# Performance work log

Measured on AMD Instinct MI355X. Metric: run time of the kernel, lower is better.

The kernel has to match this reference:

```python
import jax, jax.numpy as jnp
import numpy as np

B, T, D, H = 8, 4096, 256, 256

def setup_inputs() -> dict:
    key = jax.random.key(0)
    ks = jax.random.split(key, 6)
    scale = 1.0 / np.sqrt(D)
    return {
        "x": jax.random.normal(ks[0], (B, T, D), dtype=jnp.float32),
        "h0": jax.random.normal(ks[1], (B, H), dtype=jnp.float32),
        "Wz": jax.random.normal(ks[2], (H, D), dtype=jnp.float32) * scale,
        "bz": jax.random.normal(ks[3], (H,), dtype=jnp.float32) * scale,
        "Wh": jax.random.normal(ks[4], (H, D), dtype=jnp.float32) * scale,
        "bh": jax.random.normal(ks[5], (H,), dtype=jnp.float32) * scale,
    }

def reference(x, h0, Wz, bz, Wh, bh):
    # gate and update depend only on the input (minGRU): compute in one shot
    gate = jax.nn.sigmoid(jnp.einsum("btd,hd->bth", x, Wz) + bz)   # [B,T,H]
    update = jnp.einsum("btd,hd->bth", x, Wh) + bh                  # [B,T,H]

    def step(h, gu):
        g, u = gu
        h_new = (1.0 - g) * h + g * u
        return h_new, h_new

    # scan over time; xs laid out [T,B,H]
    _, hs = jax.lax.scan(step, h0, (jnp.swapaxes(gate, 0, 1), jnp.swapaxes(update, 0, 1)))
    return jnp.swapaxes(hs, 0, 1)  # [B,T,H]
```

## Files before the change

### kernel.cpp

```cpp
#include <hip/hip_runtime.h>
#include <hip/hip_fp16.h>


namespace {
constexpr int kB  = 8;
constexpr int kT  = 4096;
constexpr int kD  = 256;
constexpr int kH  = 256;
constexpr int kBT = kB * kT;

constexpr int TM  = 128;
constexpr int TH  = 64;
constexpr int BK  = 64;
constexpr int kNT = kT / TM;
constexpr int kNChain = kB * (kH / TH);
constexpr int EPS = 66;
}

typedef short s16x8 __attribute__((ext_vector_type(8)));
typedef short s16x4 __attribute__((ext_vector_type(4)));
typedef float f32x4 __attribute__((ext_vector_type(4)));

__device__ __forceinline__ short f2bf(float f) {
    union { float f; unsigned int u; } v; v.f = f;
    unsigned int r = v.u + 0x7fffu + ((v.u >> 16) & 1u);
    return (short)(r >> 16);
}

__device__ __forceinline__ unsigned int cvt_pk_bf16(float lo, float hi) {
    unsigned int r;
    asm("v_cvt_pk_bf16_f32 %0, %1, %2" : "=v"(r) : "v"(lo), "v"(hi));
    return r;
}

__device__ __forceinline__ void load_lds16(const void* g, void* l) {
    __builtin_amdgcn_global_load_lds(
        (const __attribute__((address_space(1))) void*)g,
        (__attribute__((address_space(3))) void*)l, 16, 0, 0);
}

__global__ __launch_bounds__(256)
void prep(const float* __restrict__ Wz,
          const float* __restrict__ Wh,
          unsigned short* __restrict__ wzb,
          unsigned short* __restrict__ whb,
          float4* __restrict__ aggz)
{
    constexpr int W4 = kH * kD / 4;
    const int i = blockIdx.x * 256 + threadIdx.x;

    if (i >= 2 * W4) {
        float4 z; z.x = 0.f; z.y = 0.f; z.z = 0.f; z.w = 0.f;
        aggz[i - 2 * W4] = z;
        return;
    }
    const float* src; unsigned short* dst; int j;
    if (i < W4) { src = Wz; dst = wzb; j = i; }
    else        { src = Wh; dst = whb; j = i - W4; }
    const float4 v = ((const float4*)src)[j];
    s16x4 p;
    p[0] = f2bf(v.x); p[1] = f2bf(v.y); p[2] = f2bf(v.z); p[3] = f2bf(v.w);
    ((s16x4*)dst)[j] = p;
}

__global__ __launch_bounds__(256, 4)
void gemm_scan_fused(const float* __restrict__ x,
                     const unsigned short* __restrict__ wzb,
                     const unsigned short* __restrict__ whb,
                     const float* __restrict__ bz,
                     const float* __restrict__ bh,
                     const float* __restrict__ h0,
                     unsigned long long* __restrict__ agg,
                     float* __restrict__ out)
{
    __shared__ __align__(16) unsigned char smem[36096];
    unsigned short* Xs  = (unsigned short*)smem;
    unsigned short* Wzs = Xs  + 128 * 64;
    unsigned short* Whs = Wzs + 64 * 64;
    __half* a_lds   = (__half*)smem;
    __half* b_lds   = a_lds + 128 * EPS;
    float2* sub_lds = (float2*)(smem + 33792);
    float*  hs_lds  = (float*)(smem + 35840);

    const int tid  = threadIdx.x;
    const int lane = tid & 63;
    const int wv   = tid >> 6;
    const int ln15 = lane & 15;
    const int quad = lane >> 4;
    const int wr0  = (wv & 1) * 64;
    const int wc0  = (wv >> 1) * 32;

    const int id  = blockIdx.x;
    const int r8  = id & 7;
    const int q   = id >> 3;
    const int cg  = q & 3;
    const int bt  = (q >> 2) * 8 + r8;
    const int b   = bt >> 5;
    const int t   = bt & 31;
    const int chain = b * 4 + cg;
    const int col0  = cg * TH;
    const int row0  = b * kT + t * TM;

    const int srow = lane >> 3;
    const int swslot = (lane & 7) ^ srow;

    f32x4 accZ[4][2] = {};
    f32x4 accU[4][2] = {};

    for (int k0 = 0; k0 < kD; k0 += BK) {
        #pragma unroll
        for (int s = 0; s < 2; ++s) {
            const int seg = wv * 2 + s;
            const int m = seg * 8 + srow;
            load_lds16(wzb + (size_t)(col0 + m) * kD + k0 + swslot * 8,
                       Wzs + seg * 512);
            load_lds16(whb + (size_t)(col0 + m) * kD + k0 + swslot * 8,
                       Whs + seg * 512);
        }
        #pragma unroll
        for (int j = 0; j < 4; ++j) {
            const int bi  = j * 256 + tid;
            const int r   = bi >> 3;
            const int blk = bi & 7;
            const float* src = x + (size_t)(row0 + r) * kD + k0 + blk * 8;
            const float4 v0 = *(const float4*)src;
            const float4 v1 = *(const float4*)(src + 4);
            union { unsigned int u[4]; s16x8 v; } pk;
            pk.u[0] = cvt_pk_bf16(v0.x, v0.y);
            pk.u[1] = cvt_pk_bf16(v0.z, v0.w);
            pk.u[2] = cvt_pk_bf16(v1.x, v1.y);
            pk.u[3] = cvt_pk_bf16(v1.z, v1.w);
            *(s16x8*)&Xs[r * 64 + ((blk ^ (r & 7)) << 3)] = pk.v;
        }
        __syncthreads();

        #pragma unroll
        for (int kk = 0; kk < BK; kk += 32) {
            const int bblk = (kk >> 3) + quad;
            s16x8 af[4], bzf[2], buf[2];
            #pragma unroll
            for (int mt = 0; mt < 4; ++mt) {
                const int r = wr0 + mt * 16 + ln15;
                af[mt] = *(const s16x8*)&Xs[r * 64 + ((bblk ^ (r & 7)) << 3)];
            }
            #pragma unroll
            for (int nt = 0; nt < 2; ++nt) {
                const int rw = wc0 + nt * 16 + ln15;
                const int so = (bblk ^ (rw & 7)) << 3;
                bzf[nt] = *(const s16x8*)&Wzs[rw * 64 + so];
                buf[nt] = *(const s16x8*)&Whs[rw * 64 + so];
            }
            #pragma unroll
            for (int mt = 0; mt < 4; ++mt) {
                #pragma unroll
                for (int nt = 0; nt < 2; ++nt) {
                    accZ[mt][nt] = __builtin_amdgcn_mfma_f32_16x16x32_bf16(
                        af[mt], bzf[nt], accZ[mt][nt], 0, 0, 0);
                    accU[mt][nt] = __builtin_amdgcn_mfma_f32_16x16x32_bf16(
                        af[mt], buf[nt], accU[mt][nt], 0, 0, 0);
                }
            }
        }
        __syncthreads();
    }

    #pragma unroll
    for (int nt = 0; nt < 2; ++nt) {
        const int col = col0 + wc0 + nt * 16 + ln15;
        const int lc  = wc0 + nt * 16 + ln15;
        const float bzv = bz[col];
        const float bhv = bh[col];
        #pragma unroll
        for (int mt = 0; mt < 4; ++mt) {
            const int rb = wr0 + mt * 16 + quad * 4;
            #pragma unroll
            for (int r = 0; r < 4; ++r) {
                const float z = accZ[mt][nt][r] + bzv;
                const float g = 1.0f / (1.0f + __expf(-z));
                const float u = accU[mt][nt][r] + bhv;
                a_lds[(rb + r) * EPS + lc] = __float2half_rn(1.0f - g);
                b_lds[(rb + r) * EPS + lc] = __float2half_rn(g * u);
            }
        }
    }
    __syncthreads();

    const int s = tid >> 6;
    const int h = tid & 63;
    {
        float A = 1.0f, Bv = 0.0f;
        #pragma unroll 8
        for (int r = s * 32; r < s * 32 + 32; ++r) {
            const float a  = __half2float(a_lds[r * EPS + h]);
            const float bb = __half2float(b_lds[r * EPS + h]);
            Bv = fmaf(a, Bv, bb);
            A *= a;
        }
        float2 o; o.x = A; o.y = Bv;
        sub_lds[s * 64 + h] = o;
    }
    __syncthreads();

    if (tid < 64) {
        float A = 1.0f, Bv = 0.0f;
        #pragma unroll
        for (int s2 = 0; s2 < 4; ++s2) {
            const float2 g = sub_lds[s2 * 64 + tid];
            Bv = fmaf(g.x, Bv, g.y);
            A *= g.x;
        }
        union { float2 f; unsigned long long u; } pk;
        pk.f.x = A; pk.f.y = Bv;
        pk.u |= 1ull;
        __hip_atomic_store(&agg[(size_t)(chain * kNT + t) * 64 + tid], pk.u,
                           __ATOMIC_RELAXED, __HIP_MEMORY_SCOPE_AGENT);

        float hs = h0[(size_t)b * kH + col0 + tid];
        for (int j0 = 0; j0 < t; j0 += 8) {
            const int nb = (t - j0 < 8) ? (t - j0) : 8;
            unsigned long long u[8];
            #pragma unroll
            for (int q2 = 0; q2 < 8; ++q2)
                if (q2 < nb)
                    u[q2] = __hip_atomic_load(
                        &agg[(size_t)(chain * kNT + j0 + q2) * 64 + tid],
                        __ATOMIC_RELAXED, __HIP_MEMORY_SCOPE_AGENT);
            #pragma unroll
            for (int q2 = 0; q2 < 8; ++q2) {
                if (q2 < nb) {
                    while (u[q2] == 0ull)
                        u[q2] = __hip_atomic_load(
                            &agg[(size_t)(chain * kNT + j0 + q2) * 64 + tid],
                            __ATOMIC_RELAXED, __HIP_MEMORY_SCOPE_AGENT);
                    union { unsigned long long u; float2 f; } qk; qk.u = u[q2];
                    hs = fmaf(qk.f.x, hs, qk.f.y);
                }
            }
        }
        hs_lds[tid] = hs;
    }
    __syncthreads();

    {
        float hv = hs_lds[h];
        #pragma unroll
        for (int s2 = 0; s2 < s; ++s2) {
            const float2 g = sub_lds[s2 * 64 + h];
            hv = fmaf(g.x, hv, g.y);
        }
        #pragma unroll 8
        for (int r = 0; r < 32; ++r) {
            const int lr = s * 32 + r;
            const float a  = __half2float(a_lds[lr * EPS + h]);
            const float bb = __half2float(b_lds[lr * EPS + h]);
            hv = fmaf(a, hv, bb);
            __builtin_nontemporal_store(hv, &out[(size_t)(row0 + lr) * kH + col0 + h]);
        }
    }
}

extern "C" void kernel_launch(void* const* d_in, const int* in_sizes, int n_in,
                              void* d_out, int out_size, void* d_ws, size_t ws_size,
                              hipStream_t stream)
{
    const float* x  = (const float*)d_in[0];
    const float* h0 = (const float*)d_in[1];
    const float* Wz = (const float*)d_in[2];
    const float* bz = (const float*)d_in[3];
    const float* Wh = (const float*)d_in[4];
    const float* bh = (const float*)d_in[5];
    float* out = (float*)d_out;

    unsigned char* ws = (unsigned char*)d_ws;
    unsigned short* wzb = (unsigned short*)ws;   ws += (size_t)kH * kD * 2;
    unsigned short* whb = (unsigned short*)ws;   ws += (size_t)kH * kD * 2;
    unsigned long long* agg = (unsigned long long*)ws;

    constexpr int PREP_ITEMS = 2 * (kH * kD / 4)
                             + kNChain * kNT * TH * 8 / 16;
    prep<<<PREP_ITEMS / 256, 256, 0, stream>>>(
        Wz, Wh, wzb, whb, (float4*)agg);
    gemm_scan_fused<<<kNChain * kNT, 256, 0, stream>>>(
        x, wzb, whb, bz, bh, h0, agg, out);
}
```

Measured before the change: 113.6 us.

## Load GEMM operands directly from global into registers, bypassing LDS staging

Removes the LDS-staged tiling of x and the bf16 weights in the fused GEMM+scan kernel. Each lane now loads its MFMA fragments straight from global memory into registers, with a register double buffer that prefetches the next k-slice while the current one is computed. This drops the __syncthreads barriers and LDS traffic, and s_setprio is raised around the MFMA block. In exchange, x rows are re-read by the waves that share them, accesses are less coalesced, register use grows, and occupancy is lowered to 3 blocks per SM.

```diff
diff --git a/kernel.cpp b/kernel.cpp
--- a/kernel.cpp
+++ b/kernel.cpp
@@ -11,7 +11,6 @@
 
 constexpr int TM  = 128;
 constexpr int TH  = 64;
-constexpr int BK  = 64;
 constexpr int kNT = kT / TM;
 constexpr int kNChain = kB * (kH / TH);
 constexpr int EPS = 66;
@@ -31,12 +30,6 @@
     unsigned int r;
     asm("v_cvt_pk_bf16_f32 %0, %1, %2" : "=v"(r) : "v"(lo), "v"(hi));
     return r;
-}
-
-__device__ __forceinline__ void load_lds16(const void* g, void* l) {
-    __builtin_amdgcn_global_load_lds(
-        (const __attribute__((address_space(1))) void*)g,
-        (__attribute__((address_space(3))) void*)l, 16, 0, 0);
 }
 
 __global__ __launch_bounds__(256)
@@ -63,7 +56,7 @@
     ((s16x4*)dst)[j] = p;
 }
 
-__global__ __launch_bounds__(256, 4)
+__global__ __launch_bounds__(256, 3)
 void gemm_scan_fused(const float* __restrict__ x,
                      const unsigned short* __restrict__ wzb,
                      const unsigned short* __restrict__ whb,
@@ -74,9 +67,6 @@
                      float* __restrict__ out)
 {
     __shared__ __align__(16) unsigned char smem[36096];
-    unsigned short* Xs  = (unsigned short*)smem;
-    unsigned short* Wzs = Xs  + 128 * 64;
-    unsigned short* Whs = Wzs + 64 * 64;
     __half* a_lds   = (__half*)smem;
     __half* b_lds   = a_lds + 128 * EPS;
     float2* sub_lds = (float2*)(smem + 33792);
@@ -101,67 +91,68 @@
     const int col0  = cg * TH;
     const int row0  = b * kT + t * TM;
 
-    const int srow = lane >> 3;
-    const int swslot = (lane & 7) ^ srow;
-
     f32x4 accZ[4][2] = {};
     f32x4 accU[4][2] = {};
 
-    for (int k0 = 0; k0 < kD; k0 += BK) {
-        #pragma unroll
-        for (int s = 0; s < 2; ++s) {
-            const int seg = wv * 2 + s;
-            const int m = seg * 8 + srow;
-            load_lds16(wzb + (size_t)(col0 + m) * kD + k0 + swslot * 8,
-                       Wzs + seg * 512);
-            load_lds16(whb + (size_t)(col0 + m) * kD + k0 + swslot * 8,
-                       Whs + seg * 512);
-        }
-        #pragma unroll
-        for (int j = 0; j < 4; ++j) {
-            const int bi  = j * 256 + tid;
-            const int r   = bi >> 3;
-            const int blk = bi & 7;
-            const float* src = x + (size_t)(row0 + r) * kD + k0 + blk * 8;
-            const float4 v0 = *(const float4*)src;
-            const float4 v1 = *(const float4*)(src + 4);
+    const float* xbase = x + (size_t)(row0 + wr0 + ln15) * kD + quad * 8;
+    const unsigned short* wzbase = wzb + (size_t)(col0 + wc0 + ln15) * kD + quad * 8;
+    const unsigned short* whbase = whb + (size_t)(col0 + wc0 + ln15) * kD + quad * 8;
+
+    float4 cxa[4], cxb[4];
+    s16x8  wzr[2][2], whr[2][2];
+
+    #pragma unroll
+    for (int mt = 0; mt < 4; ++mt) {
+        const float* p = xbase + (size_t)mt * 16 * kD;
+        cxa[mt] = *(const float4*)p;
+        cxb[mt] = *(const float4*)(p + 4);
+    }
+    #pragma unroll
+    for (int nt = 0; nt < 2; ++nt) {
+        wzr[0][nt] = *(const s16x8*)(wzbase + (size_t)nt * 16 * kD);
+        whr[0][nt] = *(const s16x8*)(whbase + (size_t)nt * 16 * kD);
+    }
+
+    #pragma unroll
+    for (int st = 0; st < 8; ++st) {
+        s16x8 af[4];
+        #pragma unroll
+        for (int mt = 0; mt < 4; ++mt) {
             union { unsigned int u[4]; s16x8 v; } pk;
-            pk.u[0] = cvt_pk_bf16(v0.x, v0.y);
-            pk.u[1] = cvt_pk_bf16(v0.z, v0.w);
-            pk.u[2] = cvt_pk_bf16(v1.x, v1.y);
-            pk.u[3] = cvt_pk_bf16(v1.z, v1.w);
-            *(s16x8*)&Xs[r * 64 + ((blk ^ (r & 7)) << 3)] = pk.v;
-        }
-        __syncthreads();
-
-        #pragma unroll
-        for (int kk = 0; kk < BK; kk += 32) {
-            const int bblk = (kk >> 3) + quad;
-            s16x8 af[4], bzf[2], buf[2];
+            pk.u[0] = cvt_pk_bf16(cxa[mt].x, cxa[mt].y);
+            pk.u[1] = cvt_pk_bf16(cxa[mt].z, cxa[mt].w);
+            pk.u[2] = cvt_pk_bf16(cxb[mt].x, cxb[mt].y);
+            pk.u[3] = cvt_pk_bf16(cxb[mt].z, cxb[mt].w);
+            af[mt] = pk.v;
+        }
+        if (st < 7) {
+            const int o = (st + 1) * 32;
             #pragma unroll
             for (int mt = 0; mt < 4; ++mt) {
-                const int r = wr0 + mt * 16 + ln15;
-                af[mt] = *(const s16x8*)&Xs[r * 64 + ((bblk ^ (r & 7)) << 3)];
+                const float* p = xbase + (size_t)mt * 16 * kD + o;
+                cxa[mt] = *(const float4*)p;
+                cxb[mt] = *(const float4*)(p + 4);
             }
             #pragma unroll
             for (int nt = 0; nt < 2; ++nt) {
-                const int rw = wc0 + nt * 16 + ln15;
-                const int so = (bblk ^ (rw & 7)) << 3;
-                bzf[nt] = *(const s16x8*)&Wzs[rw * 64 + so];
-                buf[nt] = *(const s16x8*)&Whs[rw * 64 + so];
-            }
-            #pragma unroll
-            for (int mt = 0; mt < 4; ++mt) {
-                #pragma unroll
-                for (int nt = 0; nt < 2; ++nt) {
-                    accZ[mt][nt] = __builtin_amdgcn_mfma_f32_16x16x32_bf16(
-                        af[mt], bzf[nt], accZ[mt][nt], 0, 0, 0);
-                    accU[mt][nt] = __builtin_amdgcn_mfma_f32_16x16x32_bf16(
-                        af[mt], buf[nt], accU[mt][nt], 0, 0, 0);
-                }
-            }
-        }
-        __syncthreads();
+                wzr[(st + 1) & 1][nt] =
+                    *(const s16x8*)(wzbase + (size_t)nt * 16 * kD + o);
+                whr[(st + 1) & 1][nt] =
+                    *(const s16x8*)(whbase + (size_t)nt * 16 * kD + o);
+            }
+        }
+        __builtin_amdgcn_s_setprio(1);
+        #pragma unroll
+        for (int mt = 0; mt < 4; ++mt) {
+            #pragma unroll
+            for (int nt = 0; nt < 2; ++nt) {
+                accZ[mt][nt] = __builtin_amdgcn_mfma_f32_16x16x32_bf16(
+                    af[mt], wzr[st & 1][nt], accZ[mt][nt], 0, 0, 0);
+                accU[mt][nt] = __builtin_amdgcn_mfma_f32_16x16x32_bf16(
+                    af[mt], whr[st & 1][nt], accU[mt][nt], 0, 0, 0);
+            }
+        }
+        __builtin_amdgcn_s_setprio(0);
     }
 
     #pragma unroll
```

Measured after the change: 147.3 us. +29.7%, slower.

## Halve time tile, process two tiles per block with carried state and prefetch

Applied to the files above, without the earlier changes.

Shrinks the time tile to 64 rows and has each block handle two tiles, the second being 32 tiles later in the same chain. For the second tile the block starts the serial lookback from its own first tile's result, so it only scans the tiles in between. The K loop now prefetches the next x slice into registers and double-buffers the weights in LDS, and MFMA issue gets higher wave priority. This aims to shorten the decoupled-lookback chain and overlap global loads with compute, at the cost of more barriers and larger LDS use per block.

```diff
diff --git a/kernel.cpp b/kernel.cpp
--- a/kernel.cpp
+++ b/kernel.cpp
@@ -7,13 +7,12 @@
 constexpr int kT  = 4096;
 constexpr int kD  = 256;
 constexpr int kH  = 256;
-constexpr int kBT = kB * kT;
-
-constexpr int TM  = 128;
+
+constexpr int TM  = 64;
 constexpr int TH  = 64;
 constexpr int BK  = 64;
-constexpr int kNT = kT / TM;
-constexpr int kNChain = kB * (kH / TH);
+constexpr int kTilesPC = kT / TM;
+constexpr int kNChain  = kB * (kH / TH);
 constexpr int EPS = 66;
 }
 
@@ -73,189 +72,246 @@
                      unsigned long long* __restrict__ agg,
                      float* __restrict__ out)
 {
-    __shared__ __align__(16) unsigned char smem[36096];
-    unsigned short* Xs  = (unsigned short*)smem;
-    unsigned short* Wzs = Xs  + 128 * 64;
-    unsigned short* Whs = Wzs + 64 * 64;
+    __shared__ __align__(16) unsigned char smem[40960];
+    unsigned short* Xs = (unsigned short*)smem;
     __half* a_lds   = (__half*)smem;
-    __half* b_lds   = a_lds + 128 * EPS;
-    float2* sub_lds = (float2*)(smem + 33792);
-    float*  hs_lds  = (float*)(smem + 35840);
+    __half* b_lds   = a_lds + 64 * EPS;
+    float2* sub_lds = (float2*)(smem + 16896);
+    float*  hs_lds  = (float*)(smem + 18944);
 
     const int tid  = threadIdx.x;
     const int lane = tid & 63;
     const int wv   = tid >> 6;
     const int ln15 = lane & 15;
     const int quad = lane >> 4;
-    const int wr0  = (wv & 1) * 64;
+    const int wr0  = (wv & 1) * 32;
     const int wc0  = (wv >> 1) * 32;
 
     const int id  = blockIdx.x;
     const int r8  = id & 7;
     const int q   = id >> 3;
     const int cg  = q & 3;
-    const int bt  = (q >> 2) * 8 + r8;
-    const int b   = bt >> 5;
-    const int t   = bt & 31;
+    const int idx = (q >> 2) * 8 + r8;
+    const int b   = idx >> 5;
+    const int j   = idx & 31;
     const int chain = b * 4 + cg;
     const int col0  = cg * TH;
-    const int row0  = b * kT + t * TM;
 
     const int srow = lane >> 3;
     const int swslot = (lane & 7) ^ srow;
-
-    f32x4 accZ[4][2] = {};
-    f32x4 accU[4][2] = {};
-
-    for (int k0 = 0; k0 < kD; k0 += BK) {
-        #pragma unroll
-        for (int s = 0; s < 2; ++s) {
-            const int seg = wv * 2 + s;
+    const int xr   = tid >> 3;
+    const int xblk = tid & 7;
+
+    float carry = 0.f;
+
+    for (int rnd = 0; rnd < 2; ++rnd) {
+        const int t    = j + rnd * 32;
+        const int row0 = b * kT + t * TM;
+
+        f32x4 accZ[2][2] = {};
+        f32x4 accU[2][2] = {};
+        float4 xv0[2], xv1[2];
+
+        #pragma unroll
+        for (int jj = 0; jj < 2; ++jj) {
+            const int r = jj * 32 + xr;
+            const float* p = x + (size_t)(row0 + r) * kD + xblk * 8;
+            xv0[jj] = *(const float4*)p;
+            xv1[jj] = *(const float4*)(p + 4);
+        }
+        #pragma unroll
+        for (int s2 = 0; s2 < 2; ++s2) {
+            const int seg = wv * 2 + s2;
             const int m = seg * 8 + srow;
-            load_lds16(wzb + (size_t)(col0 + m) * kD + k0 + swslot * 8,
-                       Wzs + seg * 512);
-            load_lds16(whb + (size_t)(col0 + m) * kD + k0 + swslot * 8,
-                       Whs + seg * 512);
-        }
-        #pragma unroll
-        for (int j = 0; j < 4; ++j) {
-            const int bi  = j * 256 + tid;
-            const int r   = bi >> 3;
-            const int blk = bi & 7;
-            const float* src = x + (size_t)(row0 + r) * kD + k0 + blk * 8;
-            const float4 v0 = *(const float4*)src;
-            const float4 v1 = *(const float4*)(src + 4);
+            load_lds16(wzb + (size_t)(col0 + m) * kD + swslot * 8,
+                       smem + 8192 + seg * 1024);
+            load_lds16(whb + (size_t)(col0 + m) * kD + swslot * 8,
+                       smem + 16384 + seg * 1024);
+        }
+        #pragma unroll
+        for (int jj = 0; jj < 2; ++jj) {
+            const int r = jj * 32 + xr;
             union { unsigned int u[4]; s16x8 v; } pk;
-            pk.u[0] = cvt_pk_bf16(v0.x, v0.y);
-            pk.u[1] = cvt_pk_bf16(v0.z, v0.w);
-            pk.u[2] = cvt_pk_bf16(v1.x, v1.y);
-            pk.u[3] = cvt_pk_bf16(v1.z, v1.w);
-            *(s16x8*)&Xs[r * 64 + ((blk ^ (r & 7)) << 3)] = pk.v;
-        }
-        __syncthreads();
-
-        #pragma unroll
-        for (int kk = 0; kk < BK; kk += 32) {
-            const int bblk = (kk >> 3) + quad;
-            s16x8 af[4], bzf[2], buf[2];
+            pk.u[0] = cvt_pk_bf16(xv0[jj].x, xv0[jj].y);
+            pk.u[1] = cvt_pk_bf16(xv0[jj].z, xv0[jj].w);
+            pk.u[2] = cvt_pk_bf16(xv1[jj].x, xv1[jj].y);
+            pk.u[3] = cvt_pk_bf16(xv1[jj].z, xv1[jj].w);
+            *(s16x8*)&Xs[r * 64 + ((xblk ^ (r & 7)) << 3)] = pk.v;
+        }
+        __syncthreads();
+
+        #pragma unroll
+        for (int k = 0; k < 4; ++k) {
+            if (k < 3) {
+                const int o = (k + 1) * BK;
+                #pragma unroll
+                for (int jj = 0; jj < 2; ++jj) {
+                    const int r = jj * 32 + xr;
+                    const float* p = x + (size_t)(row0 + r) * kD + o + xblk * 8;
+                    xv0[jj] = *(const float4*)p;
+                    xv1[jj] = *(const float4*)(p + 4);
+                }
+                unsigned char* wn = smem + 8192 + (((k + 1) & 1) ? 16384 : 0);
+                #pragma unroll
+                for (int s2 = 0; s2 < 2; ++s2) {
+                    const int seg = wv * 2 + s2;
+                    const int m = seg * 8 + srow;
+                    load_lds16(wzb + (size_t)(col0 + m) * kD + o + swslot * 8,
+                               wn + seg * 1024);
+                    load_lds16(whb + (size_t)(col0 + m) * kD + o + swslot * 8,
+                               wn + 8192 + seg * 1024);
+                }
+            }
+            __builtin_amdgcn_sched_barrier(0);
+
+            const unsigned short* Wzc =
+                (const unsigned short*)(smem + 8192 + ((k & 1) ? 16384 : 0));
+            const unsigned short* Whc = Wzc + 4096;
             #pragma unroll
-            for (int mt = 0; mt < 4; ++mt) {
-                const int r = wr0 + mt * 16 + ln15;
-                af[mt] = *(const s16x8*)&Xs[r * 64 + ((bblk ^ (r & 7)) << 3)];
-            }
+            for (int kk = 0; kk < BK; kk += 32) {
+                const int bblk = (kk >> 3) + quad;
+                s16x8 af[2], bzf[2], bhf[2];
+                #pragma unroll
+                for (int mt = 0; mt < 2; ++mt) {
+                    const int r = wr0 + mt * 16 + ln15;
+                    af[mt] = *(const s16x8*)&Xs[r * 64 + ((bblk ^ (r & 7)) << 3)];
+                }
+                #pragma unroll
+                for (int nt = 0; nt < 2; ++nt) {
+                    const int rw = wc0 + nt * 16 + ln15;
+                    const int so = (bblk ^ (rw & 7)) << 3;
+                    bzf[nt] = *(const s16x8*)&Wzc[rw * 64 + so];
+                    bhf[nt] = *(const s16x8*)&Whc[rw * 64 + so];
+                }
+                __builtin_amdgcn_s_setprio(1);
+                #pragma unroll
+                for (int mt = 0; mt < 2; ++mt) {
+                    #pragma unroll
+                    for (int nt = 0; nt < 2; ++nt) {
+                        accZ[mt][nt] = __builtin_amdgcn_mfma_f32_16x16x32_bf16(
+                            af[mt], bzf[nt], accZ[mt][nt], 0, 0, 0);
+                        accU[mt][nt] = __builtin_amdgcn_mfma_f32_16x16x32_bf16(
+                            af[mt], bhf[nt], accU[mt][nt], 0, 0, 0);
+                    }
+                }
+                __builtin_amdgcn_s_setprio(0);
+            }
+            __syncthreads();
+
+            if (k < 3) {
+                #pragma unroll
+                for (int jj = 0; jj < 2; ++jj) {
+                    const int r = jj * 32 + xr;
+                    union { unsigned int u[4]; s16x8 v; } pk;
+                    pk.u[0] = cvt_pk_bf16(xv0[jj].x, xv0[jj].y);
+                    pk.u[1] = cvt_pk_bf16(xv0[jj].z, xv0[jj].w);
+                    pk.u[2] = cvt_pk_bf16(xv1[jj].x, xv1[jj].y);
+                    pk.u[3] = cvt_pk_bf16(xv1[jj].z, xv1[jj].w);
+                    *(s16x8*)&Xs[r * 64 + ((xblk ^ (r & 7)) << 3)] = pk.v;
+                }
+                __syncthreads();
+            }
+        }
+
+        #pragma unroll
+        for (int nt = 0; nt < 2; ++nt) {
+            const int col = col0 + wc0 + nt * 16 + ln15;
+            const int lc  = wc0 + nt * 16 + ln15;
+            const float bzv = bz[col];
+            const float bhv = bh[col];
             #pragma unroll
-            for (int nt = 0; nt < 2; ++nt) {
-                const int rw = wc0 + nt * 16 + ln15;
-                const int so = (bblk ^ (rw & 7)) << 3;
-                bzf[nt] = *(const s16x8*)&Wzs[rw * 64 + so];
-                buf[nt] = *(const s16x8*)&Whs[rw * 64 + so];
-            }
+            for (int mt = 0; mt < 2; ++mt) {
+                const int rb = wr0 + mt * 16 + quad * 4;
+                #pragma unroll
+                for (int r = 0; r < 4; ++r) {
+                    const float z = accZ[mt][nt][r] + bzv;
+                    const float g = 1.0f / (1.0f + __expf(-z));
+                    const float u = accU[mt][nt][r] + bhv;
+                    a_lds[(rb + r) * EPS + lc] = __float2half_rn(1.0f - g);
+                    b_lds[(rb + r) * EPS + lc] = __float2half_rn(g * u);
+                }
+            }
+        }
+        __syncthreads();
+
+        const int s = tid >> 6;
+        const int h = tid & 63;
+        {
+            float A = 1.0f, Bv = 0.0f;
+            #pragma unroll 8
+            for (int r = s * 16; r < s * 16 + 16; ++r) {
+                const float a  = __half2float(a_lds[r * EPS + h]);
+                const float bb = __half2float(b_lds[r * EPS + h]);
+                Bv = fmaf(a, Bv, bb);
+                A *= a;
+            }
+            float2 o; o.x = A; o.y = Bv;
+            sub_lds[s * 64 + h] = o;
+        }
+        __syncthreads();
+
+        if (tid < 64) {
+            float A = 1.0f, Bv = 0.0f;
             #pragma unroll
-            for (int mt = 0; mt < 4; ++mt) {
-                #pragma unroll
-                for (int nt = 0; nt < 2; ++nt) {
-                    accZ[mt][nt] = __builtin_amdgcn_mfma_f32_16x16x32_bf16(
-                        af[mt], bzf[nt], accZ[mt][nt], 0, 0, 0);
-                    accU[mt][nt] = __builtin_amdgcn_mfma_f32_16x16x32_bf16(
-                        af[mt], buf[nt], accU[mt][nt], 0, 0, 0);
-                }
-            }
-        }
-        __syncthreads();
-    }
-
-    #pragma unroll
-    for (int nt = 0; nt < 2; ++nt) {
-        const int col = col0 + wc0 + nt * 16 + ln15;
-        const int lc  = wc0 + nt * 16 + ln15;
-        const float bzv = bz[col];
-        const float bhv = bh[col];
-        #pragma unroll
-        for (int mt = 0; mt < 4; ++mt) {
-            const int rb = wr0 + mt * 16 + quad * 4;
+            for (int s2 = 0; s2 < 4; ++s2) {
+                const float2 g = sub_lds[s2 * 64 + tid];
+                Bv = fmaf(g.x, Bv, g.y);
+                A *= g.x;
+            }
+            union { float2 f; unsigned long long u; } pk;
+            pk.f.x = A; pk.f.y = Bv;
+            pk.u |= 1ull;
+            __hip_atomic_store(&agg[(size_t)(chain * kTilesPC + t) * 64 + tid],
+                               pk.u, __ATOMIC_RELAXED, __HIP_MEMORY_SCOPE_AGENT);
+
+            float hs;
+            int p0;
+            if (rnd == 0) { hs = h0[(size_t)b * kH + col0 + tid]; p0 = 0; }
+            else          { hs = carry;                            p0 = j + 1; }
+            for (; p0 < t; p0 += 8) {
+                const int nb = (t - p0 < 8) ? (t - p0) : 8;
+                unsigned long long u[8];
+                #pragma unroll
+                for (int q2 = 0; q2 < 8; ++q2)
+                    if (q2 < nb)
+                        u[q2] = __hip_atomic_load(
+                            &agg[(size_t)(chain * kTilesPC + p0 + q2) * 64 + tid],
+                            __ATOMIC_RELAXED, __HIP_MEMORY_SCOPE_AGENT);
+                #pragma unroll
+                for (int q2 = 0; q2 < 8; ++q2) {
+                    if (q2 < nb) {
+                        while (u[q2] == 0ull)
+                            u[q2] = __hip_atomic_load(
+                                &agg[(size_t)(chain * kTilesPC + p0 + q2) * 64 + tid],
+                                __ATOMIC_RELAXED, __HIP_MEMORY_SCOPE_AGENT);
+                        union { unsigned long long u; float2 f; } qk; qk.u = u[q2];
+                        hs = fmaf(qk.f.x, hs, qk.f.y);
+                    }
+                }
+            }
+            hs_lds[tid] = hs;
+            if (rnd == 0) carry = fmaf(A, hs, Bv);
+        }
+        __syncthreads();
+
+        {
+            float hv = hs_lds[h];
             #pragma unroll
-            for (int r = 0; r < 4; ++r) {
-                const float z = accZ[mt][nt][r] + bzv;
-                const float g = 1.0f / (1.0f + __expf(-z));
-                const float u = accU[mt][nt][r] + bhv;
-                a_lds[(rb + r) * EPS + lc] = __float2half_rn(1.0f - g);
-                b_lds[(rb + r) * EPS + lc] = __float2half_rn(g * u);
-            }
-        }
-    }
-    __syncthreads();
-
-    const int s = tid >> 6;
-    const int h = tid & 63;
-    {
-        float A = 1.0f, Bv = 0.0f;
-        #pragma unroll 8
-        for (int r = s * 32; r < s * 32 + 32; ++r) {
-            const float a  = __half2float(a_lds[r * EPS + h]);
-            const float bb = __half2float(b_lds[r * EPS + h]);
-            Bv = fmaf(a, Bv, bb);
-            A *= a;
-        }
-        float2 o; o.x = A; o.y = Bv;
-        sub_lds[s * 64 + h] = o;
-    }
-    __syncthreads();
-
-    if (tid < 64) {
-        float A = 1.0f, Bv = 0.0f;
-        #pragma unroll
-        for (int s2 = 0; s2 < 4; ++s2) {
-            const float2 g = sub_lds[s2 * 64 + tid];
-            Bv = fmaf(g.x, Bv, g.y);
-            A *= g.x;
-        }
-        union { float2 f; unsigned long long u; } pk;
-        pk.f.x = A; pk.f.y = Bv;
-        pk.u |= 1ull;
-        __hip_atomic_store(&agg[(size_t)(chain * kNT + t) * 64 + tid], pk.u,
-                           __ATOMIC_RELAXED, __HIP_MEMORY_SCOPE_AGENT);
-
-        float hs = h0[(size_t)b * kH + col0 + tid];
-        for (int j0 = 0; j0 < t; j0 += 8) {
-            const int nb = (t - j0 < 8) ? (t - j0) : 8;
-            unsigned long long u[8];
-            #pragma unroll
-            for (int q2 = 0; q2 < 8; ++q2)
-                if (q2 < nb)
-                    u[q2] = __hip_atomic_load(
-                        &agg[(size_t)(chain * kNT + j0 + q2) * 64 + tid],
-                        __ATOMIC_RELAXED, __HIP_MEMORY_SCOPE_AGENT);
-            #pragma unroll
-            for (int q2 = 0; q2 < 8; ++q2) {
-                if (q2 < nb) {
-                    while (u[q2] == 0ull)
-                        u[q2] = __hip_atomic_load(
-                            &agg[(size_t)(chain * kNT + j0 + q2) * 64 + tid],
-                            __ATOMIC_RELAXED, __HIP_MEMORY_SCOPE_AGENT);
-                    union { unsigned long long u; float2 f; } qk; qk.u = u[q2];
-                    hs = fmaf(qk.f.x, hs, qk.f.y);
-                }
-            }
-        }
-        hs_lds[tid] = hs;
-    }
-    __syncthreads();
-
-    {
-        float hv = hs_lds[h];
-        #pragma unroll
-        for (int s2 = 0; s2 < s; ++s2) {
-            const float2 g = sub_lds[s2 * 64 + h];
-            hv = fmaf(g.x, hv, g.y);
-        }
-        #pragma unroll 8
-        for (int r = 0; r < 32; ++r) {
-            const int lr = s * 32 + r;
-            const float a  = __half2float(a_lds[lr * EPS + h]);
-            const float bb = __half2float(b_lds[lr * EPS + h]);
-            hv = fmaf(a, hv, bb);
-            __builtin_nontemporal_store(hv, &out[(size_t)(row0 + lr) * kH + col0 + h]);
-        }
+            for (int s2 = 0; s2 < s; ++s2) {
+                const float2 g = sub_lds[s2 * 64 + h];
+                hv = fmaf(g.x, hv, g.y);
+            }
+            #pragma unroll 8
+            for (int r = 0; r < 16; ++r) {
+                const int lr = s * 16 + r;
+                const float a  = __half2float(a_lds[lr * EPS + h]);
+                const float bb = __half2float(b_lds[lr * EPS + h]);
+                hv = fmaf(a, hv, bb);
+                __builtin_nontemporal_store(
+                    hv, &out[(size_t)(row0 + lr) * kH + col0 + h]);
+            }
+        }
+        __syncthreads();
     }
 }
 
@@ -277,9 +333,9 @@
     unsigned long long* agg = (unsigned long long*)ws;
 
     constexpr int PREP_ITEMS = 2 * (kH * kD / 4)
-                             + kNChain * kNT * TH * 8 / 16;
+                             + kNChain * kTilesPC * 64 * 8 / 16;
     prep<<<PREP_ITEMS / 256, 256, 0, stream>>>(
         Wz, Wh, wzb, whb, (float4*)agg);
-    gemm_scan_fused<<<kNChain * kNT, 256, 0, stream>>>(
+    gemm_scan_fused<<<kNChain * 32, 256, 0, stream>>>(
         x, wzb, whb, bz, bh, h0, agg, out);
 }
```

Result: slower. 132.8 us (+16.9%).

## Pre-convert x to bf16 in prologue and double-buffer async LDS loads in GEMM

Applied to the files above, without the earlier changes.

The prologue kernel now converts the whole input x to bf16 in workspace alongside the weights. The fused GEMM then loads x tiles straight into LDS via global_load_lds instead of doing in-kernel float loads and conversion. The K loop uses BK=32 with double-buffered LDS, prefetching the next tile while computing the current one, and raises wave priority around the MFMAs. This aims to overlap memory with compute and cut per-block conversion work. The cost is an extra full pass writing and re-reading x in bf16, which adds global traffic before the main kernel, since each x element is reused by four column-group blocks.

```diff
diff --git a/kernel.cpp b/kernel.cpp
--- a/kernel.cpp
+++ b/kernel.cpp
@@ -11,7 +11,7 @@
 
 constexpr int TM  = 128;
 constexpr int TH  = 64;
-constexpr int BK  = 64;
+constexpr int BK  = 32;
 constexpr int kNT = kT / TM;
 constexpr int kNChain = kB * (kH / TH);
 constexpr int EPS = 66;
@@ -27,12 +27,6 @@
     return (short)(r >> 16);
 }
 
-__device__ __forceinline__ unsigned int cvt_pk_bf16(float lo, float hi) {
-    unsigned int r;
-    asm("v_cvt_pk_bf16_f32 %0, %1, %2" : "=v"(r) : "v"(lo), "v"(hi));
-    return r;
-}
-
 __device__ __forceinline__ void load_lds16(const void* g, void* l) {
     __builtin_amdgcn_global_load_lds(
         (const __attribute__((address_space(1))) void*)g,
@@ -40,23 +34,27 @@
 }
 
 __global__ __launch_bounds__(256)
-void prep(const float* __restrict__ Wz,
-          const float* __restrict__ Wh,
-          unsigned short* __restrict__ wzb,
-          unsigned short* __restrict__ whb,
-          float4* __restrict__ aggz)
+void prologue(const float* __restrict__ x,
+              const float* __restrict__ Wz,
+              const float* __restrict__ Wh,
+              unsigned short* __restrict__ xbg,
+              unsigned short* __restrict__ wzb,
+              unsigned short* __restrict__ whb,
+              float4* __restrict__ aggz)
 {
-    constexpr int W4 = kH * kD / 4;
+    constexpr int X4 = kBT * kD / 4;
+    constexpr int W4 = kH  * kD / 4;
     const int i = blockIdx.x * 256 + threadIdx.x;
 
-    if (i >= 2 * W4) {
+    if (i >= X4 + 2 * W4) {
         float4 z; z.x = 0.f; z.y = 0.f; z.z = 0.f; z.w = 0.f;
-        aggz[i - 2 * W4] = z;
+        aggz[i - (X4 + 2 * W4)] = z;
         return;
     }
     const float* src; unsigned short* dst; int j;
-    if (i < W4) { src = Wz; dst = wzb; j = i; }
-    else        { src = Wh; dst = whb; j = i - W4; }
+    if (i < X4)           { src = x;  dst = xbg; j = i; }
+    else if (i < X4 + W4) { src = Wz; dst = wzb; j = i - X4; }
+    else                  { src = Wh; dst = whb; j = i - X4 - W4; }
     const float4 v = ((const float4*)src)[j];
     s16x4 p;
     p[0] = f2bf(v.x); p[1] = f2bf(v.y); p[2] = f2bf(v.z); p[3] = f2bf(v.w);
@@ -64,7 +62,7 @@
 }
 
 __global__ __launch_bounds__(256, 4)
-void gemm_scan_fused(const float* __restrict__ x,
+void gemm_scan_fused(const unsigned short* __restrict__ xbg,
                      const unsigned short* __restrict__ wzb,
                      const unsigned short* __restrict__ whb,
                      const float* __restrict__ bz,
@@ -74,9 +72,6 @@
                      float* __restrict__ out)
 {
     __shared__ __align__(16) unsigned char smem[36096];
-    unsigned short* Xs  = (unsigned short*)smem;
-    unsigned short* Wzs = Xs  + 128 * 64;
-    unsigned short* Whs = Wzs + 64 * 64;
     __half* a_lds   = (__half*)smem;
     __half* b_lds   = a_lds + 128 * EPS;
     float2* sub_lds = (float2*)(smem + 33792);
@@ -101,66 +96,73 @@
     const int col0  = cg * TH;
     const int row0  = b * kT + t * TM;
 
-    const int srow = lane >> 3;
-    const int swslot = (lane & 7) ^ srow;
+    const int xrow   = lane >> 2;
+    const int xfetch = (lane & 3) ^ (xrow & 3);
 
     f32x4 accZ[4][2] = {};
     f32x4 accU[4][2] = {};
 
-    for (int k0 = 0; k0 < kD; k0 += BK) {
-        #pragma unroll
-        for (int s = 0; s < 2; ++s) {
-            const int seg = wv * 2 + s;
-            const int m = seg * 8 + srow;
-            load_lds16(wzb + (size_t)(col0 + m) * kD + k0 + swslot * 8,
-                       Wzs + seg * 512);
-            load_lds16(whb + (size_t)(col0 + m) * kD + k0 + swslot * 8,
-                       Whs + seg * 512);
-        }
-        #pragma unroll
-        for (int j = 0; j < 4; ++j) {
-            const int bi  = j * 256 + tid;
-            const int r   = bi >> 3;
-            const int blk = bi & 7;
-            const float* src = x + (size_t)(row0 + r) * kD + k0 + blk * 8;
-            const float4 v0 = *(const float4*)src;
-            const float4 v1 = *(const float4*)(src + 4);
-            union { unsigned int u[4]; s16x8 v; } pk;
-            pk.u[0] = cvt_pk_bf16(v0.x, v0.y);
-            pk.u[1] = cvt_pk_bf16(v0.z, v0.w);
-            pk.u[2] = cvt_pk_bf16(v1.x, v1.y);
-            pk.u[3] = cvt_pk_bf16(v1.z, v1.w);
-            *(s16x8*)&Xs[r * 64 + ((blk ^ (r & 7)) << 3)] = pk.v;
-        }
-        __syncthreads();
-
-        #pragma unroll
-        for (int kk = 0; kk < BK; kk += 32) {
-            const int bblk = (kk >> 3) + quad;
-            s16x8 af[4], bzf[2], buf[2];
-            #pragma unroll
-            for (int mt = 0; mt < 4; ++mt) {
-                const int r = wr0 + mt * 16 + ln15;
-                af[mt] = *(const s16x8*)&Xs[r * 64 + ((bblk ^ (r & 7)) << 3)];
-            }
+    #pragma unroll
+    for (int s2 = 0; s2 < 2; ++s2) {
+        const int seg = wv * 2 + s2;
+        load_lds16(xbg + (size_t)(row0 + seg * 16 + xrow) * kD + xfetch * 8,
+                   smem + seg * 1024);
+    }
+    load_lds16(wzb + (size_t)(col0 + wv * 16 + xrow) * kD + xfetch * 8,
+               smem + 16384 + wv * 1024);
+    load_lds16(whb + (size_t)(col0 + wv * 16 + xrow) * kD + xfetch * 8,
+               smem + 20480 + wv * 1024);
+    __syncthreads();
+
+    #pragma unroll
+    for (int k = 0; k < 8; ++k) {
+        const int cur = k & 1;
+        if (k < 7) {
+            const int o  = (k + 1) * BK;
+            const int nb = cur ^ 1;
+            #pragma unroll
+            for (int s2 = 0; s2 < 2; ++s2) {
+                const int seg = wv * 2 + s2;
+                load_lds16(
+                    xbg + (size_t)(row0 + seg * 16 + xrow) * kD + o + xfetch * 8,
+                    smem + nb * 8192 + seg * 1024);
+            }
+            load_lds16(wzb + (size_t)(col0 + wv * 16 + xrow) * kD + o + xfetch * 8,
+                       smem + 16384 + nb * 8192 + wv * 1024);
+            load_lds16(whb + (size_t)(col0 + wv * 16 + xrow) * kD + o + xfetch * 8,
+                       smem + 16384 + nb * 8192 + 4096 + wv * 1024);
+        }
+        __builtin_amdgcn_sched_barrier(0);
+
+        const unsigned short* Xc  = (const unsigned short*)(smem + cur * 8192);
+        const unsigned short* Wzc = (const unsigned short*)(smem + 16384 + cur * 8192);
+        const unsigned short* Whc = Wzc + 2048;
+
+        s16x8 af[4], bzf[2], bhf[2];
+        #pragma unroll
+        for (int mt = 0; mt < 4; ++mt) {
+            const int r = wr0 + mt * 16 + ln15;
+            af[mt] = *(const s16x8*)&Xc[r * 32 + ((quad ^ (r & 3)) << 3)];
+        }
+        #pragma unroll
+        for (int nt = 0; nt < 2; ++nt) {
+            const int rw = wc0 + nt * 16 + ln15;
+            const int so = (quad ^ (rw & 3)) << 3;
+            bzf[nt] = *(const s16x8*)&Wzc[rw * 32 + so];
+            bhf[nt] = *(const s16x8*)&Whc[rw * 32 + so];
+        }
+        __builtin_amdgcn_s_setprio(1);
+        #pragma unroll
+        for (int mt = 0; mt < 4; ++mt) {
             #pragma unroll
             for (int nt = 0; nt < 2; ++nt) {
-                const int rw = wc0 + nt * 16 + ln15;
-                const int so = (bblk ^ (rw & 7)) << 3;
-                bzf[nt] = *(const s16x8*)&Wzs[rw * 64 + so];
-                buf[nt] = *(const s16x8*)&Whs[rw * 64 + so];
-            }
-            #pragma unroll
-            for (int mt = 0; mt < 4; ++mt) {
-                #pragma unroll
-                for (int nt = 0; nt < 2; ++nt) {
-                    accZ[mt][nt] = __builtin_amdgcn_mfma_f32_16x16x32_bf16(
-                        af[mt], bzf[nt], accZ[mt][nt], 0, 0, 0);
-                    accU[mt][nt] = __builtin_amdgcn_mfma_f32_16x16x32_bf16(
-                        af[mt], buf[nt], accU[mt][nt], 0, 0, 0);
-                }
-            }
-        }
+                accZ[mt][nt] = __builtin_amdgcn_mfma_f32_16x16x32_bf16(
+                    af[mt], bzf[nt], accZ[mt][nt], 0, 0, 0);
+                accU[mt][nt] = __builtin_amdgcn_mfma_f32_16x16x32_bf16(
+                    af[mt], bhf[nt], accU[mt][nt], 0, 0, 0);
+            }
+        }
+        __builtin_amdgcn_s_setprio(0);
         __syncthreads();
     }
 
@@ -272,14 +274,15 @@
     float* out = (float*)d_out;
 
     unsigned char* ws = (unsigned char*)d_ws;
+    unsigned short* xbg = (unsigned short*)ws;   ws += (size_t)kBT * kD * 2;
     unsigned short* wzb = (unsigned short*)ws;   ws += (size_t)kH * kD * 2;
     unsigned short* whb = (unsigned short*)ws;   ws += (size_t)kH * kD * 2;
     unsigned long long* agg = (unsigned long long*)ws;
 
-    constexpr int PREP_ITEMS = 2 * (kH * kD / 4)
-                             + kNChain * kNT * TH * 8 / 16;
-    prep<<<PREP_ITEMS / 256, 256, 0, stream>>>(
-        Wz, Wh, wzb, whb, (float4*)agg);
+    constexpr int PRO_ITEMS = kBT * kD / 4 + 2 * (kH * kD / 4)
+                            + kNChain * kNT * TH * 8 / 16;
+    prologue<<<PRO_ITEMS / 256, 256, 0, stream>>>(
+        x, Wz, Wh, xbg, wzb, whb, (float4*)agg);
     gemm_scan_fused<<<kNChain * kNT, 256, 0, stream>>>(
-        x, wzb, whb, bz, bh, h0, agg, out);
-}
+        xbg, wzb, whb, bz, bh, h0, agg, out);
+}
```

New measurement: 114.8 us. No clear change (+1.1%).
